# Kernel tuning notes

Measured on AMD Instinct MI355X. Metric: run time of the kernel, lower is better.

Reference implementation:

```python
import jax, jax.numpy as jnp
import numpy as np

B, T, D = 2, 2048, 1024   # batch, seq, d_model
E, K, H = 8, 2, 704       # routed experts, topk, expert hidden
SH = 704 * 2              # shared-expert hidden = moe_hidden * num_shared_experts
EPS = 1e-20               # topk_norm_epsilon
STD = 0.02                # init_weight_std


def setup_inputs() -> dict:
    key = jax.random.key(0)
    ks = jax.random.split(key, 8)
    return {
        "x":   jax.random.normal(ks[0], (B, T, D), jnp.float32),
        "Wg":  jax.random.normal(ks[1], (E, D), jnp.float32) * STD,   # router experts_weights
        "W1":  jax.random.normal(ks[2], (E, D, H), jnp.float32) * STD,  # gate proj per expert
        "W3":  jax.random.normal(ks[3], (E, D, H), jnp.float32) * STD,  # up proj per expert
        "W2":  jax.random.normal(ks[4], (E, H, D), jnp.float32) * STD,  # down proj per expert
        "Ws1": jax.random.normal(ks[5], (D, SH), jnp.float32) * STD,    # shared expert
        "Ws3": jax.random.normal(ks[6], (D, SH), jnp.float32) * STD,
        "Ws2": jax.random.normal(ks[7], (SH, D), jnp.float32) * STD,
    }


def reference(x, Wg, W1, W3, W2, Ws1, Ws3, Ws2):
    b, t, d = x.shape
    n = b * t
    xf = x.reshape(n, d)
    # softmax gating + topk + scatter back into dense [N,E] gate matrix
    gates = jax.nn.softmax(xf @ Wg.T, axis=-1)                      # [N,E]
    top_v, top_i = jax.lax.top_k(gates, K)                          # [N,K]
    masked = jnp.zeros_like(gates).at[jnp.arange(n)[:, None], top_i].set(top_v)
    masked = masked / (masked.sum(-1, keepdims=True) + EPS)         # normalized_moe_gates
    # per-expert SwiGLU FFN over all tokens, then gate-weighted combine
    h = jnp.einsum('nd,edh->enh', xf, W1)                           # [E,N,H]
    g = jnp.einsum('nd,edh->enh', xf, W3)
    y = jnp.einsum('enh,ehd->end', jax.nn.silu(h) * g, W2)          # [E,N,D]
    routed = jnp.einsum('ne,end->nd', masked, y)                    # combine
    shared = (jax.nn.silu(xf @ Ws1) * (xf @ Ws3)) @ Ws2             # shared experts
    return (routed + shared).reshape(b, t, d)
```

## Files before the change

### kernel.cpp

```cpp
#include <hip/hip_runtime.h>
#include <math.h>

typedef __bf16 bf16;
typedef __attribute__((ext_vector_type(8))) __bf16 bf16x8;
typedef __attribute__((ext_vector_type(4))) __bf16 bf16x4;
typedef __attribute__((ext_vector_type(4))) float f32x4;

#define NTOK 4096
#define DM   1024
#define NE   8
#define HE   704
#define HS   1408

#define OFF_CNT   0u
#define OFF_TOK   256u
#define OFF_WGT   131328u
#define OFF_XB    262400u
#define OFF_W1T   8651008u
#define OFF_W3T   20185344u
#define OFF_W2T   31719680u
#define OFF_WS1T  43254016u
#define OFF_WS3T  46137600u
#define OFF_WS2T  49021184u
#define OFF_ACTR  51904768u
#define OFF_ACTS  63439104u
#define OFF_EIDS  74973440u
#define OFF_GW    74989824u

__device__ __forceinline__ void async_cp16(const bf16* g, bf16* l)
{
    __builtin_amdgcn_global_load_lds(
        (const __attribute__((address_space(1))) unsigned int*)g,
        (__attribute__((address_space(3))) unsigned int*)l, 16, 0, 0);
}

__global__ void cvt_x_kernel(const float* __restrict__ x, bf16* __restrict__ xb, int n4)
{
    int i = blockIdx.x * blockDim.x + threadIdx.x;
    if (i >= n4) return;
    float4 v = ((const float4*)x)[i];
    bf16x4 o;
    o[0] = (bf16)v.x; o[1] = (bf16)v.y; o[2] = (bf16)v.z; o[3] = (bf16)v.w;
    ((bf16x4*)xb)[i] = o;
}

__global__ void transpose_cvt(const float* __restrict__ src, bf16* __restrict__ dst, int R, int C)
{
    __shared__ float t[32][33];
    int c0 = blockIdx.x * 32, r0 = blockIdx.y * 32;
    size_t base = (size_t)blockIdx.z * (size_t)R * (size_t)C;
    src += base; dst += base;
    int row  = threadIdx.x >> 3;
    int col4 = (threadIdx.x & 7) * 4;
    float4 v = *(const float4*)&src[(size_t)(r0 + row) * C + c0 + col4];
    t[row][col4 + 0] = v.x; t[row][col4 + 1] = v.y;
    t[row][col4 + 2] = v.z; t[row][col4 + 3] = v.w;
    __syncthreads();
    bf16x4 o;
    o[0] = (bf16)t[col4 + 0][row];
    o[1] = (bf16)t[col4 + 1][row];
    o[2] = (bf16)t[col4 + 2][row];
    o[3] = (bf16)t[col4 + 3][row];
    *(bf16x4*)&dst[(size_t)(c0 + row) * R + r0 + col4] = o;
}

__global__ __launch_bounds__(256) void router_logits(
    const float* __restrict__ x, const float* __restrict__ Wg,
    int* __restrict__ eids, float2* __restrict__ gw)
{
    int n    = blockIdx.x * 4 + (threadIdx.x >> 6);
    int lane = threadIdx.x & 63;
    const float* xrow = x + (size_t)n * DM;
    float xr[16];
    #pragma unroll
    for (int j = 0; j < 16; j++) xr[j] = xrow[lane + 64 * j];
    float logit[NE];
    #pragma unroll
    for (int e = 0; e < NE; e++) {
        const float* wr = Wg + e * DM;
        float s = 0.f;
        #pragma unroll
        for (int j = 0; j < 16; j++) s += xr[j] * wr[lane + 64 * j];
        #pragma unroll
        for (int off = 32; off; off >>= 1) s += __shfl_xor(s, off, 64);
        logit[e] = s;
    }
    if (lane == 0) {
        int i0 = 0;
        #pragma unroll
        for (int e = 1; e < NE; e++) if (logit[e] > logit[i0]) i0 = e;
        int i1 = (i0 == 0) ? 1 : 0;
        #pragma unroll
        for (int e = 0; e < NE; e++) if (e != i0 && logit[e] > logit[i1]) i1 = e;
        float m = logit[0];
        #pragma unroll
        for (int e = 1; e < NE; e++) m = fmaxf(m, logit[e]);
        float denom = 0.f;
        #pragma unroll
        for (int e = 0; e < NE; e++) denom += expf(logit[e] - m);
        float g0 = expf(logit[i0] - m) / denom;
        float g1 = expf(logit[i1] - m) / denom;
        float inv = 1.f / (g0 + g1 + 1e-20f);
        eids[n] = i0 | (i1 << 16);
        gw[n] = make_float2(g0 * inv, g1 * inv);
    }
}

__global__ __launch_bounds__(128) void build_lists(
    const int* __restrict__ eids, const float2* __restrict__ gw,
    int* __restrict__ cnt, int* __restrict__ tok, float* __restrict__ wgt)
{
    __shared__ int lcnt[NE];
    __shared__ int gbase[NE];
    int t = threadIdx.x;
    int n = blockIdx.x * 128 + t;
    if (t < NE) lcnt[t] = 0;
    __syncthreads();
    int packed = eids[n];
    float2 w = gw[n];
    int e0 = packed & 0xffff, e1 = packed >> 16;
    int s0 = atomicAdd(&lcnt[e0], 1);
    int s1 = atomicAdd(&lcnt[e1], 1);
    __syncthreads();
    if (t < NE) gbase[t] = atomicAdd(&cnt[t], lcnt[t]);
    __syncthreads();
    int p0 = gbase[e0] + s0, p1 = gbase[e1] + s1;
    tok[e0 * NTOK + p0] = n; wgt[e0 * NTOK + p0] = w.x;
    tok[e1 * NTOK + p1] = n; wgt[e1 * NTOK + p1] = w.y;
}

__global__ void prefix_kernel(const int* __restrict__ cnt, int* __restrict__ pfx)
{
    if (threadIdx.x == 0) {
        int s = 0;
        for (int e = 0; e < NE; e++) { pfx[e] = s; s += cnt[e]; }
        pfx[NE] = s;
    }
}

__global__ __launch_bounds__(256) void gemm1_swiglu(
    const bf16* __restrict__ xb,
    const bf16* __restrict__ W1t, const bf16* __restrict__ W3t,
    bf16* __restrict__ act,
    const int* __restrict__ cnt, const int* __restrict__ pfx, const int* __restrict__ tok,
    int Hdim)
{
    int e = blockIdx.z;
    int count = cnt ? cnt[e] : NTOK;
    int m0 = blockIdx.y * 128;
    if (m0 >= count) return;
    int h0 = blockIdx.x * 64;
    int base = pfx ? pfx[e] : 0;
    const bf16* B1 = W1t + (size_t)e * Hdim * DM;
    const bf16* B3 = W3t + (size_t)e * Hdim * DM;
    const int* tlist = tok ? tok + e * NTOK : nullptr;

    __shared__ bf16 As[128 * 32];
    __shared__ bf16 B1s[64 * 32];
    __shared__ bf16 B3s[64 * 32];

    int tid = threadIdx.x, w = tid >> 6, lane = tid & 63;
    int lrow4 = lane >> 2;
    int lcol8 = (lane & 3) * 8;

    int sA0 = m0 + 32 * w + lrow4;
    int sA1 = sA0 + 16;
    int rA0 = tlist ? (sA0 < count ? tlist[sA0] : 0) : (sA0 < count ? sA0 : 0);
    int rA1 = tlist ? (sA1 < count ? tlist[sA1] : 0) : (sA1 < count ? sA1 : 0);
    const bf16* ga0 = xb + (size_t)rA0 * DM + lcol8;
    const bf16* ga1 = xb + (size_t)rA1 * DM + lcol8;
    const bf16* gb1 = B1 + (size_t)(h0 + 16 * w + lrow4) * DM + lcol8;
    const bf16* gb3 = B3 + (size_t)(h0 + 16 * w + lrow4) * DM + lcol8;
    bf16* lA0 = As + 1024 * w;
    bf16* lA1 = As + 1024 * w + 512;
    bf16* lB1 = B1s + 512 * w;
    bf16* lB3 = B3s + 512 * w;

    int wm = (w & 1) * 64, wn = (w >> 1) * 32;
    int lm = lane & 15, lk = (lane >> 4) * 8;

    f32x4 acch[4][2], accg[4][2];
    #pragma unroll
    for (int i = 0; i < 4; i++)
        #pragma unroll
        for (int j = 0; j < 2; j++) {
            acch[i][j] = (f32x4){0.f, 0.f, 0.f, 0.f};
            accg[i][j] = (f32x4){0.f, 0.f, 0.f, 0.f};
        }

    for (int k0 = 0; k0 < DM; k0 += 32) {
        async_cp16(ga0, lA0);
        async_cp16(ga1, lA1);
        async_cp16(gb1, lB1);
        async_cp16(gb3, lB3);
        ga0 += 32; ga1 += 32; gb1 += 32; gb3 += 32;
        __syncthreads();
        bf16x8 af[4], b1f[2], b3f[2];
        #pragma unroll
        for (int i = 0; i < 4; i++) af[i] = *(const bf16x8*)&As[(wm + i * 16 + lm) * 32 + lk];
        #pragma unroll
        for (int j = 0; j < 2; j++) {
            b1f[j] = *(const bf16x8*)&B1s[(wn + j * 16 + lm) * 32 + lk];
            b3f[j] = *(const bf16x8*)&B3s[(wn + j * 16 + lm) * 32 + lk];
        }
        #pragma unroll
        for (int i = 0; i < 4; i++)
            #pragma unroll
            for (int j = 0; j < 2; j++) {
                acch[i][j] = __builtin_amdgcn_mfma_f32_16x16x32_bf16(af[i], b1f[j], acch[i][j], 0, 0, 0);
                accg[i][j] = __builtin_amdgcn_mfma_f32_16x16x32_bf16(af[i], b3f[j], accg[i][j], 0, 0, 0);
            }
        __syncthreads();
    }

    int quad = lane >> 4;
    #pragma unroll
    for (int i = 0; i < 4; i++)
        #pragma unroll
        for (int j = 0; j < 2; j++)
            #pragma unroll
            for (int r = 0; r < 4; r++) {
                int row = wm + i * 16 + quad * 4 + r;
                int s2 = m0 + row;
                if (s2 < count) {
                    float hv = acch[i][j][r], gv = accg[i][j][r];
                    float a = hv / (1.f + expf(-hv)) * gv;
                    act[(size_t)(base + s2) * Hdim + h0 + wn + j * 16 + lm] = (bf16)a;
                }
            }
}

__global__ __launch_bounds__(256) void gemm2_combine(
    const bf16* __restrict__ act,
    const bf16* __restrict__ W2t,
    float* __restrict__ out,
    const int* __restrict__ cnt, const int* __restrict__ pfx,
    const int* __restrict__ tok, const float* __restrict__ wgt,
    int Hdim, int atomic_mode)
{
    int e = blockIdx.z;
    int count = cnt ? cnt[e] : NTOK;
    int m0 = blockIdx.y * 128;
    if (m0 >= count) return;
    int d0 = blockIdx.x * 128;
    int base = pfx ? pfx[e] : 0;
    const bf16* B = W2t + (size_t)e * DM * Hdim;

    __shared__ bf16 As[128 * 32];
    __shared__ bf16 Bs[128 * 32];

    int tid = threadIdx.x, w = tid >> 6, lane = tid & 63;
    int lrow4 = lane >> 2;
    int lcol8 = (lane & 3) * 8;

    int sA0 = m0 + 32 * w + lrow4;
    int sA1 = sA0 + 16;
    int arow0 = (sA0 < count) ? (base + sA0) : base;
    int arow1 = (sA1 < count) ? (base + sA1) : base;
    const bf16* ga0 = act + (size_t)arow0 * Hdim + lcol8;
    const bf16* ga1 = act + (size_t)arow1 * Hdim + lcol8;
    const bf16* gb0 = B + (size_t)(d0 + 32 * w + lrow4) * Hdim + lcol8;
    const bf16* gb1 = gb0 + (size_t)16 * Hdim;
    bf16* lA0 = As + 1024 * w;
    bf16* lA1 = As + 1024 * w + 512;
    bf16* lB0 = Bs + 1024 * w;
    bf16* lB1 = Bs + 1024 * w + 512;

    int wm = (w & 1) * 64, wn = (w >> 1) * 64;
    int lm = lane & 15, lk = (lane >> 4) * 8;

    f32x4 acc[4][4];
    #pragma unroll
    for (int i = 0; i < 4; i++)
        #pragma unroll
        for (int j = 0; j < 4; j++) acc[i][j] = (f32x4){0.f, 0.f, 0.f, 0.f};

    for (int k0 = 0; k0 < Hdim; k0 += 32) {
        async_cp16(ga0, lA0);
        async_cp16(ga1, lA1);
        async_cp16(gb0, lB0);
        async_cp16(gb1, lB1);
        ga0 += 32; ga1 += 32; gb0 += 32; gb1 += 32;
        __syncthreads();
        bf16x8 af[4], bf_[4];
        #pragma unroll
        for (int i = 0; i < 4; i++) af[i]  = *(const bf16x8*)&As[(wm + i * 16 + lm) * 32 + lk];
        #pragma unroll
        for (int j = 0; j < 4; j++) bf_[j] = *(const bf16x8*)&Bs[(wn + j * 16 + lm) * 32 + lk];
        #pragma unroll
        for (int i = 0; i < 4; i++)
            #pragma unroll
            for (int j = 0; j < 4; j++)
                acc[i][j] = __builtin_amdgcn_mfma_f32_16x16x32_bf16(af[i], bf_[j], acc[i][j], 0, 0, 0);
        __syncthreads();
    }

    int quad = lane >> 4;
    #pragma unroll
    for (int i = 0; i < 4; i++)
        #pragma unroll
        for (int j = 0; j < 4; j++)
            #pragma unroll
            for (int r = 0; r < 4; r++) {
                int row = wm + i * 16 + quad * 4 + r;
                int s2 = m0 + row;
                if (s2 < count) {
                    int col = d0 + wn + j * 16 + lm;
                    float v = acc[i][j][r];
                    if (atomic_mode) {
                        int t = tok[e * NTOK + s2];
                        float wt = wgt[e * NTOK + s2];
                        atomicAdd(&out[(size_t)t * DM + col], wt * v);
                    } else {
                        out[(size_t)s2 * DM + col] = v;
                    }
                }
            }
}

extern "C" void kernel_launch(void* const* d_in, const int* in_sizes, int n_in,
                              void* d_out, int out_size, void* d_ws, size_t ws_size,
                              hipStream_t stream)
{
    const float* x   = (const float*)d_in[0];
    const float* Wg  = (const float*)d_in[1];
    const float* W1  = (const float*)d_in[2];
    const float* W3  = (const float*)d_in[3];
    const float* W2  = (const float*)d_in[4];
    const float* Ws1 = (const float*)d_in[5];
    const float* Ws3 = (const float*)d_in[6];
    const float* Ws2 = (const float*)d_in[7];
    float* out = (float*)d_out;
    char*  ws  = (char*)d_ws;

    int*    cnt  = (int*)(ws + OFF_CNT);
    int*    pfx  = (int*)(ws + OFF_CNT + 32);
    int*    tok  = (int*)(ws + OFF_TOK);
    float*  wgt  = (float*)(ws + OFF_WGT);
    bf16*   xb   = (bf16*)(ws + OFF_XB);
    bf16*   w1t  = (bf16*)(ws + OFF_W1T);
    bf16*   w3t  = (bf16*)(ws + OFF_W3T);
    bf16*   w2t  = (bf16*)(ws + OFF_W2T);
    bf16*   ws1t = (bf16*)(ws + OFF_WS1T);
    bf16*   ws3t = (bf16*)(ws + OFF_WS3T);
    bf16*   ws2t = (bf16*)(ws + OFF_WS2T);
    bf16*   actr = (bf16*)(ws + OFF_ACTR);
    bf16*   acts = (bf16*)(ws + OFF_ACTS);
    int*    eids = (int*)(ws + OFF_EIDS);
    float2* gw   = (float2*)(ws + OFF_GW);

    hipMemsetAsync(ws, 0, 256, stream);

    cvt_x_kernel<<<4096, 256, 0, stream>>>(x, xb, NTOK * DM / 4);

    transpose_cvt<<<dim3(22, 32, 8), 256, 0, stream>>>(W1,  w1t,  1024, 704);
    transpose_cvt<<<dim3(22, 32, 8), 256, 0, stream>>>(W3,  w3t,  1024, 704);
    transpose_cvt<<<dim3(32, 22, 8), 256, 0, stream>>>(W2,  w2t,  704, 1024);
    transpose_cvt<<<dim3(44, 32, 1), 256, 0, stream>>>(Ws1, ws1t, 1024, 1408);
    transpose_cvt<<<dim3(44, 32, 1), 256, 0, stream>>>(Ws3, ws3t, 1024, 1408);
    transpose_cvt<<<dim3(32, 44, 1), 256, 0, stream>>>(Ws2, ws2t, 1408, 1024);

    router_logits<<<1024, 256, 0, stream>>>(x, Wg, eids, gw);
    build_lists<<<32, 128, 0, stream>>>(eids, gw, cnt, tok, wgt);
    prefix_kernel<<<1, 64, 0, stream>>>(cnt, pfx);

    gemm1_swiglu<<<dim3(HE / 64, 32, NE), 256, 0, stream>>>(xb, w1t, w3t, actr, cnt, pfx, tok, HE);
    gemm1_swiglu<<<dim3(HS / 64, 32, 1), 256, 0, stream>>>(xb, ws1t, ws3t, acts, nullptr, nullptr, nullptr, HS);
    gemm2_combine<<<dim3(DM / 128, 32, 1), 256, 0, stream>>>(acts, ws2t, out, nullptr, nullptr, nullptr, nullptr, HS, 0);
    gemm2_combine<<<dim3(DM / 128, 32, NE), 256, 0, stream>>>(actr, w2t, out, cnt, pfx, tok, wgt, HE, 1);
}
```

Measured before the change: 367.5 us.

## Merge shared expert into grouped GEMMs, fuse transposes, use conflict-free LDS layout

The shared expert is split into two 704-wide pseudo-experts, so the routed and shared work each run in a single grouped launch for gemm1 and for gemm2. The six weight-transpose launches become one transpose_all kernel. The LDS tiles switch to a lane-contiguous sub-tile layout that matches the MFMA operand fragments, which is meant to avoid bank conflicts on fragment reads, and the grid order now puts the token tile in blockIdx.x. In exchange the output needs a full memset, and the shared expert now accumulates with atomics instead of plain stores.

```diff
diff --git a/kernel.cpp b/kernel.cpp
--- a/kernel.cpp
+++ b/kernel.cpp
@@ -9,8 +9,8 @@
 #define NTOK 4096
 #define DM   1024
 #define NE   8
+#define NEX  10
 #define HE   704
-#define HS   1408
 
 #define OFF_CNT   0u
 #define OFF_TOK   256u
@@ -22,8 +22,7 @@
 #define OFF_WS1T  43254016u
 #define OFF_WS3T  46137600u
 #define OFF_WS2T  49021184u
-#define OFF_ACTR  51904768u
-#define OFF_ACTS  63439104u
+#define OFF_ACT   51904768u
 #define OFF_EIDS  74973440u
 #define OFF_GW    74989824u
 
@@ -44,23 +43,37 @@
     ((bf16x4*)xb)[i] = o;
 }
 
-__global__ void transpose_cvt(const float* __restrict__ src, bf16* __restrict__ dst, int R, int C)
-{
-    __shared__ float t[32][33];
-    int c0 = blockIdx.x * 32, r0 = blockIdx.y * 32;
-    size_t base = (size_t)blockIdx.z * (size_t)R * (size_t)C;
-    src += base; dst += base;
+__global__ __launch_bounds__(256) void transpose_all(
+    const float* __restrict__ W1, const float* __restrict__ W3, const float* __restrict__ W2,
+    const float* __restrict__ Ws1, const float* __restrict__ Ws3, const float* __restrict__ Ws2,
+    bf16* __restrict__ w1t, bf16* __restrict__ w3t, bf16* __restrict__ w2t,
+    bf16* __restrict__ ws1t, bf16* __restrict__ ws3t, bf16* __restrict__ ws2t)
+{
+    int id = blockIdx.x;
+    const float* src; bf16* dst; int R, C, rt, ct;
+    if (id < 5632)       { int t = id;         int e = t / 704, m = t % 704; R = 1024; C = 704;
+                           src = W1 + (size_t)e * R * C;  dst = w1t + (size_t)e * R * C;  ct = m % 22; rt = m / 22; }
+    else if (id < 11264) { int t = id - 5632;  int e = t / 704, m = t % 704; R = 1024; C = 704;
+                           src = W3 + (size_t)e * R * C;  dst = w3t + (size_t)e * R * C;  ct = m % 22; rt = m / 22; }
+    else if (id < 16896) { int t = id - 11264; int e = t / 704, m = t % 704; R = 704;  C = 1024;
+                           src = W2 + (size_t)e * R * C;  dst = w2t + (size_t)e * R * C;  ct = m % 32; rt = m / 32; }
+    else if (id < 18304) { int t = id - 16896; R = 1024; C = 1408; src = Ws1; dst = ws1t; ct = t % 44; rt = t / 44; }
+    else if (id < 19712) { int t = id - 18304; R = 1024; C = 1408; src = Ws3; dst = ws3t; ct = t % 44; rt = t / 44; }
+    else                 { int t = id - 19712; R = 1408; C = 1024; src = Ws2; dst = ws2t; ct = t % 32; rt = t / 32; }
+
+    __shared__ float tl[32][33];
+    int c0 = ct * 32, r0 = rt * 32;
     int row  = threadIdx.x >> 3;
     int col4 = (threadIdx.x & 7) * 4;
     float4 v = *(const float4*)&src[(size_t)(r0 + row) * C + c0 + col4];
-    t[row][col4 + 0] = v.x; t[row][col4 + 1] = v.y;
-    t[row][col4 + 2] = v.z; t[row][col4 + 3] = v.w;
+    tl[row][col4 + 0] = v.x; tl[row][col4 + 1] = v.y;
+    tl[row][col4 + 2] = v.z; tl[row][col4 + 3] = v.w;
     __syncthreads();
     bf16x4 o;
-    o[0] = (bf16)t[col4 + 0][row];
-    o[1] = (bf16)t[col4 + 1][row];
-    o[2] = (bf16)t[col4 + 2][row];
-    o[3] = (bf16)t[col4 + 3][row];
+    o[0] = (bf16)tl[col4 + 0][row];
+    o[1] = (bf16)tl[col4 + 1][row];
+    o[2] = (bf16)tl[col4 + 2][row];
+    o[3] = (bf16)tl[col4 + 3][row];
     *(bf16x4*)&dst[(size_t)(c0 + row) * R + r0 + col4] = o;
 }
 
@@ -133,51 +146,51 @@
 {
     if (threadIdx.x == 0) {
         int s = 0;
-        for (int e = 0; e < NE; e++) { pfx[e] = s; s += cnt[e]; }
-        pfx[NE] = s;
+        for (int e = 0; e < NEX; e++) { pfx[e] = s; s += (e < NE) ? cnt[e] : NTOK; }
+        pfx[NEX] = s;
     }
 }
 
 __global__ __launch_bounds__(256) void gemm1_swiglu(
     const bf16* __restrict__ xb,
-    const bf16* __restrict__ W1t, const bf16* __restrict__ W3t,
+    const bf16* __restrict__ w1t, const bf16* __restrict__ w3t,
+    const bf16* __restrict__ ws1t, const bf16* __restrict__ ws3t,
     bf16* __restrict__ act,
-    const int* __restrict__ cnt, const int* __restrict__ pfx, const int* __restrict__ tok,
-    int Hdim)
+    const int* __restrict__ cnt, const int* __restrict__ pfx, const int* __restrict__ tok)
 {
     int e = blockIdx.z;
-    int count = cnt ? cnt[e] : NTOK;
-    int m0 = blockIdx.y * 128;
+    int count = (e < NE) ? cnt[e] : NTOK;
+    int m0 = blockIdx.x * 128;
     if (m0 >= count) return;
-    int h0 = blockIdx.x * 64;
-    int base = pfx ? pfx[e] : 0;
-    const bf16* B1 = W1t + (size_t)e * Hdim * DM;
-    const bf16* B3 = W3t + (size_t)e * Hdim * DM;
-    const int* tlist = tok ? tok + e * NTOK : nullptr;
+    int h0 = blockIdx.y * 64;
+    int base = pfx[e];
+    const bf16 *B1, *B3;
+    if (e < NE) { B1 = w1t + (size_t)e * HE * DM;        B3 = w3t + (size_t)e * HE * DM; }
+    else        { B1 = ws1t + (size_t)(e - NE) * HE * DM; B3 = ws3t + (size_t)(e - NE) * HE * DM; }
+    const int* tlist = (e < NE) ? tok + e * NTOK : nullptr;
 
     __shared__ bf16 As[128 * 32];
     __shared__ bf16 B1s[64 * 32];
     __shared__ bf16 B3s[64 * 32];
 
     int tid = threadIdx.x, w = tid >> 6, lane = tid & 63;
-    int lrow4 = lane >> 2;
-    int lcol8 = (lane & 3) * 8;
-
-    int sA0 = m0 + 32 * w + lrow4;
-    int sA1 = sA0 + 16;
+    int rl = lane & 15, ch = lane >> 4;
+
+    int sA0 = m0 + 32 * w + rl, sA1 = sA0 + 16;
     int rA0 = tlist ? (sA0 < count ? tlist[sA0] : 0) : (sA0 < count ? sA0 : 0);
     int rA1 = tlist ? (sA1 < count ? tlist[sA1] : 0) : (sA1 < count ? sA1 : 0);
-    const bf16* ga0 = xb + (size_t)rA0 * DM + lcol8;
-    const bf16* ga1 = xb + (size_t)rA1 * DM + lcol8;
-    const bf16* gb1 = B1 + (size_t)(h0 + 16 * w + lrow4) * DM + lcol8;
-    const bf16* gb3 = B3 + (size_t)(h0 + 16 * w + lrow4) * DM + lcol8;
-    bf16* lA0 = As + 1024 * w;
-    bf16* lA1 = As + 1024 * w + 512;
-    bf16* lB1 = B1s + 512 * w;
-    bf16* lB3 = B3s + 512 * w;
-
+    const bf16* ga0 = xb + (size_t)rA0 * DM + ch * 8;
+    const bf16* ga1 = xb + (size_t)rA1 * DM + ch * 8;
+    const bf16* gb1 = B1 + (size_t)(h0 + 16 * w + rl) * DM + ch * 8;
+    const bf16* gb3 = B3 + (size_t)(h0 + 16 * w + rl) * DM + ch * 8;
+    bf16* lA0 = As + (2 * w) * 512;
+    bf16* lA1 = As + (2 * w + 1) * 512;
+    bf16* lB1 = B1s + w * 512;
+    bf16* lB3 = B3s + w * 512;
+
+    int gA = (w & 1) * 4;
+    int gB = (w >> 1) * 2;
     int wm = (w & 1) * 64, wn = (w >> 1) * 32;
-    int lm = lane & 15, lk = (lane >> 4) * 8;
 
     f32x4 acch[4][2], accg[4][2];
     #pragma unroll
@@ -197,11 +210,11 @@
         __syncthreads();
         bf16x8 af[4], b1f[2], b3f[2];
         #pragma unroll
-        for (int i = 0; i < 4; i++) af[i] = *(const bf16x8*)&As[(wm + i * 16 + lm) * 32 + lk];
+        for (int i = 0; i < 4; i++) af[i] = *(const bf16x8*)(As + (gA + i) * 512 + lane * 8);
         #pragma unroll
         for (int j = 0; j < 2; j++) {
-            b1f[j] = *(const bf16x8*)&B1s[(wn + j * 16 + lm) * 32 + lk];
-            b3f[j] = *(const bf16x8*)&B3s[(wn + j * 16 + lm) * 32 + lk];
+            b1f[j] = *(const bf16x8*)(B1s + (gB + j) * 512 + lane * 8);
+            b3f[j] = *(const bf16x8*)(B3s + (gB + j) * 512 + lane * 8);
         }
         #pragma unroll
         for (int i = 0; i < 4; i++)
@@ -213,61 +226,61 @@
         __syncthreads();
     }
 
-    int quad = lane >> 4;
     #pragma unroll
     for (int i = 0; i < 4; i++)
         #pragma unroll
         for (int j = 0; j < 2; j++)
             #pragma unroll
             for (int r = 0; r < 4; r++) {
-                int row = wm + i * 16 + quad * 4 + r;
+                int row = wm + i * 16 + ch * 4 + r;
                 int s2 = m0 + row;
                 if (s2 < count) {
                     float hv = acch[i][j][r], gv = accg[i][j][r];
                     float a = hv / (1.f + expf(-hv)) * gv;
-                    act[(size_t)(base + s2) * Hdim + h0 + wn + j * 16 + lm] = (bf16)a;
+                    act[(size_t)(base + s2) * HE + h0 + wn + j * 16 + rl] = (bf16)a;
                 }
             }
 }
 
 __global__ __launch_bounds__(256) void gemm2_combine(
     const bf16* __restrict__ act,
-    const bf16* __restrict__ W2t,
+    const bf16* __restrict__ w2t, const bf16* __restrict__ ws2t,
     float* __restrict__ out,
     const int* __restrict__ cnt, const int* __restrict__ pfx,
-    const int* __restrict__ tok, const float* __restrict__ wgt,
-    int Hdim, int atomic_mode)
+    const int* __restrict__ tok, const float* __restrict__ wgt)
 {
     int e = blockIdx.z;
-    int count = cnt ? cnt[e] : NTOK;
-    int m0 = blockIdx.y * 128;
+    int count = (e < NE) ? cnt[e] : NTOK;
+    int m0 = blockIdx.x * 128;
     if (m0 >= count) return;
-    int d0 = blockIdx.x * 128;
-    int base = pfx ? pfx[e] : 0;
-    const bf16* B = W2t + (size_t)e * DM * Hdim;
+    int d0 = blockIdx.y * 128;
+    int base = pfx[e];
+    const bf16* B; size_t ldB;
+    if (e < NE) { B = w2t + (size_t)e * DM * HE; ldB = HE; }
+    else        { B = ws2t + (size_t)(e - NE) * HE; ldB = 2 * HE; }
+    const int*   tlist = (e < NE) ? tok + e * NTOK : nullptr;
+    const float* wl    = (e < NE) ? wgt + e * NTOK : nullptr;
 
     __shared__ bf16 As[128 * 32];
     __shared__ bf16 Bs[128 * 32];
 
     int tid = threadIdx.x, w = tid >> 6, lane = tid & 63;
-    int lrow4 = lane >> 2;
-    int lcol8 = (lane & 3) * 8;
-
-    int sA0 = m0 + 32 * w + lrow4;
-    int sA1 = sA0 + 16;
-    int arow0 = (sA0 < count) ? (base + sA0) : base;
-    int arow1 = (sA1 < count) ? (base + sA1) : base;
-    const bf16* ga0 = act + (size_t)arow0 * Hdim + lcol8;
-    const bf16* ga1 = act + (size_t)arow1 * Hdim + lcol8;
-    const bf16* gb0 = B + (size_t)(d0 + 32 * w + lrow4) * Hdim + lcol8;
-    const bf16* gb1 = gb0 + (size_t)16 * Hdim;
-    bf16* lA0 = As + 1024 * w;
-    bf16* lA1 = As + 1024 * w + 512;
-    bf16* lB0 = Bs + 1024 * w;
-    bf16* lB1 = Bs + 1024 * w + 512;
-
+    int rl = lane & 15, ch = lane >> 4;
+
+    int sA0 = m0 + 32 * w + rl, sA1 = sA0 + 16;
+    int a0 = (sA0 < count) ? (base + sA0) : base;
+    int a1 = (sA1 < count) ? (base + sA1) : base;
+    const bf16* ga0 = act + (size_t)a0 * HE + ch * 8;
+    const bf16* ga1 = act + (size_t)a1 * HE + ch * 8;
+    const bf16* gb0 = B + (size_t)(d0 + 32 * w + rl) * ldB + ch * 8;
+    const bf16* gb1 = B + (size_t)(d0 + 32 * w + 16 + rl) * ldB + ch * 8;
+    bf16* lA0 = As + (2 * w) * 512;
+    bf16* lA1 = As + (2 * w + 1) * 512;
+    bf16* lB0 = Bs + (2 * w) * 512;
+    bf16* lB1 = Bs + (2 * w + 1) * 512;
+
+    int gA = (w & 1) * 4, gB = (w >> 1) * 4;
     int wm = (w & 1) * 64, wn = (w >> 1) * 64;
-    int lm = lane & 15, lk = (lane >> 4) * 8;
 
     f32x4 acc[4][4];
     #pragma unroll
@@ -275,7 +288,7 @@
         #pragma unroll
         for (int j = 0; j < 4; j++) acc[i][j] = (f32x4){0.f, 0.f, 0.f, 0.f};
 
-    for (int k0 = 0; k0 < Hdim; k0 += 32) {
+    for (int k0 = 0; k0 < HE; k0 += 32) {
         async_cp16(ga0, lA0);
         async_cp16(ga1, lA1);
         async_cp16(gb0, lB0);
@@ -284,9 +297,9 @@
         __syncthreads();
         bf16x8 af[4], bf_[4];
         #pragma unroll
-        for (int i = 0; i < 4; i++) af[i]  = *(const bf16x8*)&As[(wm + i * 16 + lm) * 32 + lk];
-        #pragma unroll
-        for (int j = 0; j < 4; j++) bf_[j] = *(const bf16x8*)&Bs[(wn + j * 16 + lm) * 32 + lk];
+        for (int i = 0; i < 4; i++) af[i]  = *(const bf16x8*)(As + (gA + i) * 512 + lane * 8);
+        #pragma unroll
+        for (int j = 0; j < 4; j++) bf_[j] = *(const bf16x8*)(Bs + (gB + j) * 512 + lane * 8);
         #pragma unroll
         for (int i = 0; i < 4; i++)
             #pragma unroll
@@ -295,25 +308,19 @@
         __syncthreads();
     }
 
-    int quad = lane >> 4;
     #pragma unroll
     for (int i = 0; i < 4; i++)
         #pragma unroll
         for (int j = 0; j < 4; j++)
             #pragma unroll
             for (int r = 0; r < 4; r++) {
-                int row = wm + i * 16 + quad * 4 + r;
+                int row = wm + i * 16 + ch * 4 + r;
                 int s2 = m0 + row;
                 if (s2 < count) {
-                    int col = d0 + wn + j * 16 + lm;
-                    float v = acc[i][j][r];
-                    if (atomic_mode) {
-                        int t = tok[e * NTOK + s2];
-                        float wt = wgt[e * NTOK + s2];
-                        atomicAdd(&out[(size_t)t * DM + col], wt * v);
-                    } else {
-                        out[(size_t)s2 * DM + col] = v;
-                    }
+                    int   t  = tlist ? tlist[s2] : s2;
+                    float wt = wl ? wl[s2] : 1.0f;
+                    int col = d0 + wn + j * 16 + rl;
+                    atomicAdd(&out[(size_t)t * DM + col], wt * acc[i][j][r]);
                 }
             }
 }
@@ -344,28 +351,22 @@
     bf16*   ws1t = (bf16*)(ws + OFF_WS1T);
     bf16*   ws3t = (bf16*)(ws + OFF_WS3T);
     bf16*   ws2t = (bf16*)(ws + OFF_WS2T);
-    bf16*   actr = (bf16*)(ws + OFF_ACTR);
-    bf16*   acts = (bf16*)(ws + OFF_ACTS);
+    bf16*   act  = (bf16*)(ws + OFF_ACT);
     int*    eids = (int*)(ws + OFF_EIDS);
     float2* gw   = (float2*)(ws + OFF_GW);
 
     hipMemsetAsync(ws, 0, 256, stream);
+    hipMemsetAsync(out, 0, (size_t)NTOK * DM * sizeof(float), stream);
 
     cvt_x_kernel<<<4096, 256, 0, stream>>>(x, xb, NTOK * DM / 4);
-
-    transpose_cvt<<<dim3(22, 32, 8), 256, 0, stream>>>(W1,  w1t,  1024, 704);
-    transpose_cvt<<<dim3(22, 32, 8), 256, 0, stream>>>(W3,  w3t,  1024, 704);
-    transpose_cvt<<<dim3(32, 22, 8), 256, 0, stream>>>(W2,  w2t,  704, 1024);
-    transpose_cvt<<<dim3(44, 32, 1), 256, 0, stream>>>(Ws1, ws1t, 1024, 1408);
-    transpose_cvt<<<dim3(44, 32, 1), 256, 0, stream>>>(Ws3, ws3t, 1024, 1408);
-    transpose_cvt<<<dim3(32, 44, 1), 256, 0, stream>>>(Ws2, ws2t, 1408, 1024);
-
+    transpose_all<<<21120, 256, 0, stream>>>(W1, W3, W2, Ws1, Ws3, Ws2,
+                                             w1t, w3t, w2t, ws1t, ws3t, ws2t);
     router_logits<<<1024, 256, 0, stream>>>(x, Wg, eids, gw);
     build_lists<<<32, 128, 0, stream>>>(eids, gw, cnt, tok, wgt);
     prefix_kernel<<<1, 64, 0, stream>>>(cnt, pfx);
 
-    gemm1_swiglu<<<dim3(HE / 64, 32, NE), 256, 0, stream>>>(xb, w1t, w3t, actr, cnt, pfx, tok, HE);
-    gemm1_swiglu<<<dim3(HS / 64, 32, 1), 256, 0, stream>>>(xb, ws1t, ws3t, acts, nullptr, nullptr, nullptr, HS);
-    gemm2_combine<<<dim3(DM / 128, 32, 1), 256, 0, stream>>>(acts, ws2t, out, nullptr, nullptr, nullptr, nullptr, HS, 0);
-    gemm2_combine<<<dim3(DM / 128, 32, NE), 256, 0, stream>>>(actr, w2t, out, cnt, pfx, tok, wgt, HE, 1);
-}
+    gemm1_swiglu<<<dim3(32, HE / 64, NEX), 256, 0, stream>>>(
+        xb, w1t, w3t, ws1t, ws3t, act, cnt, pfx, tok);
+    gemm2_combine<<<dim3(32, DM / 128, NEX), 256, 0, stream>>>(
+        act, w2t, ws2t, out, cnt, pfx, tok, wgt);
+}
```

New measurement: 589.8 us. +60.5%, slower.
